# Kernel optimization log

Measured on AMD Instinct MI355X. Metric: run time of the kernel, lower is better.

The kernel has to match this reference:

```python
import jax, jax.numpy as jnp
import numpy as np

N_NODES, N_EDGES, N_GRAPHS = 100000, 1600000, 1000
DIN, DMID, DGLOB, DOUT = 128, 128, 64, 2


def setup_inputs() -> dict:
    key = jax.random.key(0)
    ks = jax.random.split(key, 12)
    x = jax.random.normal(ks[0], (N_NODES, DIN), dtype=jnp.float32)
    edge_index = jax.random.randint(ks[1], (2, N_EDGES), 0, N_NODES, dtype=jnp.int64 if jax.config.jax_enable_x64 else jnp.int32)
    u = jax.random.normal(ks[2], (N_GRAPHS, DGLOB), dtype=jnp.float32)
    batch = jnp.sort(jax.random.randint(ks[3], (N_NODES,), 0, N_GRAPHS))
    s = 1.0 / np.sqrt(DMID)
    W1 = jax.random.normal(ks[4], (DIN, DMID), dtype=jnp.float32) * s
    b1 = jnp.zeros((DMID,), dtype=jnp.float32)
    W2 = jax.random.normal(ks[5], (DMID, DMID), dtype=jnp.float32) * s
    b2 = jnp.zeros((DMID,), dtype=jnp.float32)
    Wh1 = jax.random.normal(ks[6], (DMID + DGLOB, DMID), dtype=jnp.float32) * s
    bh1 = jnp.zeros((DMID,), dtype=jnp.float32)
    Wh2 = jax.random.normal(ks[7], (DMID, DOUT), dtype=jnp.float32) * s
    bh2 = jnp.zeros((DOUT,), dtype=jnp.float32)
    return {"x": x, "edge_index": edge_index, "u": u, "batch": batch,
            "batch_size": N_GRAPHS, "W1": W1, "b1": b1, "W2": W2, "b2": b2,
            "Wh1": Wh1, "bh1": bh1, "Wh2": Wh2, "bh2": bh2}


def _gcn_conv(x, W, b, row, col, norm, n):
    # PyG GCNConv: linear transform then symmetric-normalized scatter-add
    h = x @ W                                    # [N, dmid]
    msg = norm[:, None] * h[row]                 # gather along source nodes
    out = jax.ops.segment_sum(msg, col, num_segments=n)  # scatter to dst
    return out + b


def reference(x, edge_index, u, batch, batch_size, W1, b1, W2, b2, Wh1, bh1, Wh2, bh2):
    n = x.shape[0]
    # add self-loops (GCNConv default, edge_weight=None -> all-ones weights)
    loop = jnp.arange(n, dtype=edge_index.dtype)
    row = jnp.concatenate([edge_index[0], loop])
    col = jnp.concatenate([edge_index[1], loop])
    deg = jax.ops.segment_sum(jnp.ones_like(col, dtype=x.dtype), col, num_segments=n)
    dinv = jnp.where(deg > 0, jax.lax.rsqrt(jnp.maximum(deg, 1e-12)), 0.0)
    norm = dinv[row] * dinv[col]                 # D^-1/2 A D^-1/2, shared by both layers

    h = jax.nn.relu(_gcn_conv(x, W1, b1, row, col, norm, n))
    h = jax.nn.relu(_gcn_conv(h, W2, b2, row, col, norm, n))

    # mean pool per graph
    sums = jax.ops.segment_sum(h, batch, num_segments=batch_size)
    cnt = jax.ops.segment_sum(jnp.ones((n,), dtype=h.dtype), batch, num_segments=batch_size)
    graph_emb = sums / jnp.maximum(cnt, 1.0)[:, None]

    hcat = jnp.concatenate([graph_emb, u], axis=-1)
    # head MLP (dropout in eval mode = identity)
    out = jax.nn.relu(hcat @ Wh1 + bh1) @ Wh2 + bh2
    return out
```

## Files before the change

### kernel.cpp

```cpp
#include <hip/hip_runtime.h>
#include <hip/hip_bf16.h>

#define NN 100000
#define NE 1600000
#define NG 1000
#define NBK 196
#define BSH 9
#define SLOT 10240
#define SLOTC 12288

typedef short short8 __attribute__((ext_vector_type(8)));
typedef float f32x4 __attribute__((ext_vector_type(4)));
typedef float f32x2 __attribute__((ext_vector_type(2)));

static inline int cdiv(int a, int b) { return (a + b - 1) / b; }

__device__ __forceinline__ unsigned short f2b(float f) {
    unsigned int u = __float_as_uint(f);
    u += 0x7fff + ((u >> 16) & 1);
    return (unsigned short)(u >> 16);
}
__device__ __forceinline__ unsigned int pack2(float lo, float hi) {
    return (unsigned int)f2b(lo) | ((unsigned int)f2b(hi) << 16);
}

template <int W>
__device__ __forceinline__ f32x2 f8_2f(unsigned int v) {
    return __builtin_amdgcn_cvt_pk_f32_fp8((int)v, W);
}
__device__ __forceinline__ unsigned int f2f8_lo(float a, float b, unsigned int old) {
    return (unsigned int)__builtin_amdgcn_cvt_pk_fp8_f32(a, b, (int)old, false);
}
__device__ __forceinline__ unsigned int f2f8_hi(float a, float b, unsigned int old) {
    return (unsigned int)__builtin_amdgcn_cvt_pk_fp8_f32(a, b, (int)old, true);
}
__device__ __forceinline__ unsigned char f2f8s(float a) {
    return (unsigned char)(__builtin_amdgcn_cvt_pk_fp8_f32(a, a, 0, false) & 0xFF);
}

__global__ __launch_bounds__(256) void k_prep(const float* __restrict__ W1,
                                              const float* __restrict__ W2,
                                              const float* __restrict__ b1,
                                              const float* __restrict__ b2,
                                              unsigned short* __restrict__ Wt1,
                                              unsigned char* __restrict__ Wt2p,
                                              float* __restrict__ b1p,
                                              float* __restrict__ b2p,
                                              int* __restrict__ gcur,
                                              const int* __restrict__ batch,
                                              int* __restrict__ gstart,
                                              unsigned char* __restrict__ Hs8,
                                              unsigned char* __restrict__ Hg2) {
    int b = blockIdx.x, t = threadIdx.x;
    if (b < 128) {
        if (t < 128) {
            Wt1[b * 128 + t] = f2b(W1[t * 128 + b]);
        } else {
            int q = t - 128;
            int c = (q & 7) * 16 + (q >> 3);
            Wt2p[b * 128 + q] = f2f8s(W2[c * 128 + b]);
        }
    } else if (b == 128) {
        if (t < NBK) gcur[t] = t * SLOT;
        if (t < 128) {
            int c = (t & 7) * 16 + (t >> 3);
            b1p[t] = b1[c];
            b2p[t] = b2[c];
        }
        if (t >= 128 && t < 136) {
            uint4 z; z.x = 0u; z.y = 0u; z.z = 0u; z.w = 0u;
            ((uint4*)(Hs8 + (size_t)NN * 128))[t - 128] = z;
        }
        if (t >= 136 && t < 144) {
            uint4 z; z.x = 0u; z.y = 0u; z.z = 0u; z.w = 0u;
            ((uint4*)(Hg2 + (size_t)NN * 128))[t - 136] = z;
        }
    } else {
        int n = (b - 129) * 256 + t;
        if (n <= NN) {
            int cur = (n == NN) ? NG : batch[n];
            int prev = (n == 0) ? -1 : batch[n - 1];
            for (int g = prev + 1; g <= cur; g++) gstart[g] = n;
        }
    }
}

__global__ __launch_bounds__(256) void k_bin2(const int* __restrict__ row,
                                              const int* __restrict__ col,
                                              int* __restrict__ gcur,
                                              unsigned int* __restrict__ tmp) {
    __shared__ unsigned int ent[4000];
    __shared__ unsigned int srt[4000];
    __shared__ unsigned char bkt[4000];
    __shared__ unsigned char bky[4000];
    __shared__ int cnt[NBK];
    __shared__ int gbase[NBK];
    __shared__ int lbase[NBK];
    __shared__ int sh[256];
    int t = threadIdx.x;
    if (t < NBK) cnt[t] = 0;
    __syncthreads();
    const int q0 = blockIdx.x * 1000;
    const int4* col4 = (const int4*)col;
    const int4* row4 = (const int4*)row;
#pragma unroll
    for (int it = 0; it < 4; it++) {
        int idx = it * 256 + t;
        if (idx < 1000) {
            int4 c = col4[q0 + idx];
            int4 r = row4[q0 + idx];
            int d, b;
            d = c.x; b = d >> BSH; atomicAdd(&cnt[b], 1);
            ent[idx * 4 + 0] = ((unsigned int)(d & 511) << 17) | (unsigned int)r.x;
            bkt[idx * 4 + 0] = (unsigned char)b;
            d = c.y; b = d >> BSH; atomicAdd(&cnt[b], 1);
            ent[idx * 4 + 1] = ((unsigned int)(d & 511) << 17) | (unsigned int)r.y;
            bkt[idx * 4 + 1] = (unsigned char)b;
            d = c.z; b = d >> BSH; atomicAdd(&cnt[b], 1);
            ent[idx * 4 + 2] = ((unsigned int)(d & 511) << 17) | (unsigned int)r.z;
            bkt[idx * 4 + 2] = (unsigned char)b;
            d = c.w; b = d >> BSH; atomicAdd(&cnt[b], 1);
            ent[idx * 4 + 3] = ((unsigned int)(d & 511) << 17) | (unsigned int)r.w;
            bkt[idx * 4 + 3] = (unsigned char)b;
        }
    }
    __syncthreads();
    int v = (t < NBK) ? cnt[t] : 0;
    sh[t] = v;
    __syncthreads();
    for (int d = 1; d < 256; d <<= 1) {
        int u = (t >= d) ? sh[t - d] : 0;
        __syncthreads();
        sh[t] += u;
        __syncthreads();
    }
    if (t < NBK) {
        lbase[t] = sh[t] - v;
        gbase[t] = atomicAdd(&gcur[t], v);
        cnt[t] = sh[t] - v;
    }
    __syncthreads();
#pragma unroll
    for (int it = 0; it < 16; it++) {
        int i = it * 256 + t;
        if (i < 4000) {
            int b = bkt[i];
            int p = atomicAdd(&cnt[b], 1);
            srt[p] = ent[i];
            bky[p] = (unsigned char)b;
        }
    }
    __syncthreads();
#pragma unroll
    for (int it = 0; it < 16; it++) {
        int i = it * 256 + t;
        if (i < 4000) {
            int b = bky[i];
            tmp[gbase[b] + (i - lbase[b])] = srt[i];
        }
    }
}

__global__ __launch_bounds__(1024) void k_bucket(const unsigned int* __restrict__ tmp,
                                                 const int* __restrict__ gcur,
                                                 unsigned int* __restrict__ meta,
                                                 float* __restrict__ dinv,
                                                 int* __restrict__ csr_src) {
    __shared__ unsigned int sent[SLOT];
    __shared__ int cnt[512];
    __shared__ int loff[512];
    __shared__ int send[512];
    __shared__ int sh[256];
    int b = blockIdx.x, t = threadIdx.x;
    int j0 = b << BSH;
    int nd = min(512, NN - j0);
    int rb = b * SLOT;
    int rbc = b * SLOTC;
    int m = gcur[b] - rb;
    if (t < 512) cnt[t] = 0;
    __syncthreads();
    for (int i = t; i < m; i += 1024) {
        unsigned int e = tmp[rb + i];
        sent[i] = e;
        atomicAdd(&cnt[e >> 17], 1);
    }
    __syncthreads();
    int r0 = 0, r1 = 0, p0 = 0, ts = 0;
    if (t < 256) {
        r0 = cnt[2 * t]; r1 = cnt[2 * t + 1];
        p0 = (r0 + 7) & ~7;
        int p1 = (r1 + 7) & ~7;
        ts = p0 + p1;
        sh[t] = ts;
    }
    __syncthreads();
    for (int d = 1; d < 256; d <<= 1) {
        int u = (t >= d && t < 256) ? sh[t - d] : 0;
        __syncthreads();
        if (t < 256) sh[t] += u;
        __syncthreads();
    }
    if (t < 256) {
        int ex = sh[t] - ts;
        loff[2 * t] = ex;
        loff[2 * t + 1] = ex + p0;
    }
    __syncthreads();
    for (int j = t; j < nd; j += 1024) {
        int o = rbc + loff[j];
        int dg = cnt[j];
        int dgp = (dg + 7) & ~7;
        meta[j0 + j] = (unsigned int)o | ((unsigned int)dgp << 22);
        send[j] = o + dgp;
        dinv[j0 + j] = rsqrtf((float)(dg + 1));
        cnt[j] = o;
    }
    __syncthreads();
    for (int i = t; i < m; i += 1024) {
        unsigned int e = sent[i];
        int d = e >> 17;
        int s = (int)(e & 0x1FFFFu);
        int p = atomicAdd(&cnt[d], 1);
        csr_src[p] = s;
    }
    __syncthreads();
    for (int j = t; j < nd; j += 1024) {
        int pe = send[j];
        for (int p = cnt[j]; p < pe; p++) csr_src[p] = NN;
    }
}

__global__ __launch_bounds__(256) void k_gemm1(const float* __restrict__ X,
                                               const unsigned short* __restrict__ Wt,
                                               const float* __restrict__ dinv,
                                               unsigned char* __restrict__ Hs8) {
    __shared__ __align__(16) unsigned short Ws[128 * 128];
    int t = threadIdx.x;
#pragma unroll
    for (int i = 0; i < 8; i++) {
        int id = t + i * 256;
        int n = id >> 4, c = id & 15;
        *(short8*)((char*)Ws + n * 256 + ((c ^ (n & 15)) << 4)) =
            *(const short8*)(Wt + n * 128 + c * 8);
    }
    __syncthreads();

    int lane = t & 63, wid = t >> 6;
    int n16 = lane & 15, quad = lane >> 4;
    int row_base = blockIdx.x * 128 + wid * 32;

    short8 a[2][4];
#pragma unroll
    for (int rt = 0; rt < 2; rt++) {
        int r = row_base + rt * 16 + n16;
        if (r > NN - 1) r = NN - 1;
        const float* ap = X + (size_t)r * 128 + quad * 8;
#pragma unroll
        for (int ks = 0; ks < 4; ks++) {
            float4 v0 = *(const float4*)(ap + ks * 32);
            float4 v1 = *(const float4*)(ap + ks * 32 + 4);
            uint4 up;
            up.x = pack2(v0.x, v0.y); up.y = pack2(v0.z, v0.w);
            up.z = pack2(v1.x, v1.y); up.w = pack2(v1.z, v1.w);
            a[rt][ks] = *(short8*)&up;
        }
    }

    f32x4 acc[2][8];
#pragma unroll
    for (int rt = 0; rt < 2; rt++)
#pragma unroll
        for (int ct = 0; ct < 8; ct++)
            acc[rt][ct] = (f32x4){0.f, 0.f, 0.f, 0.f};

#pragma unroll
    for (int ks = 0; ks < 4; ks++) {
#pragma unroll
        for (int ct = 0; ct < 8; ct++) {
            short8 b = *(const short8*)((const char*)Ws +
                        (ct * 16 + n16) * 256 + ((((ks << 2) + quad) ^ n16) << 4));
            acc[0][ct] = __builtin_amdgcn_mfma_f32_16x16x32_bf16(a[0][ks], b, acc[0][ct], 0, 0, 0);
            acc[1][ct] = __builtin_amdgcn_mfma_f32_16x16x32_bf16(a[1][ks], b, acc[1][ct], 0, 0, 0);
        }
    }

#pragma unroll
    for (int rt = 0; rt < 2; rt++) {
#pragma unroll
        for (int reg = 0; reg < 4; reg++) {
            int row = row_base + rt * 16 + quad * 4 + reg;
            if (row < NN) {
                float di = dinv[row];
                unsigned int u0 = 0, u1 = 0;
                u0 = f2f8_lo(acc[rt][0][reg] * di, acc[rt][1][reg] * di, u0);
                u0 = f2f8_hi(acc[rt][2][reg] * di, acc[rt][3][reg] * di, u0);
                u1 = f2f8_lo(acc[rt][4][reg] * di, acc[rt][5][reg] * di, u1);
                u1 = f2f8_hi(acc[rt][6][reg] * di, acc[rt][7][reg] * di, u1);
                uint2 o; o.x = u0; o.y = u1;
                ((uint2*)(Hs8 + (size_t)row * 128))[n16] = o;
            }
        }
    }
}

template <int FUSE>
__global__ __launch_bounds__(256) void k_agg(const unsigned char* __restrict__ Hb,
                                             const unsigned int* __restrict__ meta,
                                             const int* __restrict__ csr_src,
                                             const float* __restrict__ dinv,
                                             const float* __restrict__ biasp,
                                             const unsigned char* __restrict__ Wt2p,
                                             unsigned char* __restrict__ outp) {
    __shared__ __align__(16) unsigned char sm[FUSE ? (128 * 128 + 16 * 128) : 16];
    int t = threadIdx.x;
    if (FUSE) {
#pragma unroll
        for (int i = 0; i < 8; i++) {
            int id = t + i * 256;
            int n = id >> 4, c = id & 15;
            *(uint2*)(sm + n * 128 + ((c ^ (n & 15)) << 3)) =
                *(const uint2*)(Wt2p + n * 128 + c * 8);
        }
    }
    int sub = t >> 4;
    int node = blockIdx.x * 16 + sub;
    int li = t & 15;
    unsigned lo8 = (unsigned)li * 8u;
    unsigned int md = meta[node];
    int base = (int)(md & 0x3FFFFFu);
    int degp = (int)(md >> 22);
    f32x2 A0 = {0.f, 0.f}, A1 = {0.f, 0.f}, A2 = {0.f, 0.f}, A3 = {0.f, 0.f};
#define LDH(idx) (*(const uint2*)(Hb + (unsigned)(idx) * 128u + lo8))
#define ACC8(V) { \
        A0 += f8_2f<0>((V).x); A1 += f8_2f<1>((V).x); \
        A2 += f8_2f<0>((V).y); A3 += f8_2f<1>((V).y); }
    uint2 v = LDH(node);
    const int4* ip = (const int4*)(csr_src + base);
    int4 i0 = ip[0], i1 = ip[1], i2 = ip[2], i3 = ip[3];
    ACC8(v)
    for (int e0 = 0; e0 < degp; e0 += 16) {
        uint2 w0 = LDH(i0.x), w1 = LDH(i0.y), w2 = LDH(i0.z), w3 = LDH(i0.w);
        uint2 w4 = LDH(i1.x), w5 = LDH(i1.y), w6 = LDH(i1.z), w7 = LDH(i1.w);
        uint2 w8 = {0, 0}, w9 = {0, 0}, wA = {0, 0}, wB = {0, 0};
        uint2 wC = {0, 0}, wD = {0, 0}, wE = {0, 0}, wF = {0, 0};
        if (e0 + 8 < degp) {
            w8 = LDH(i2.x); w9 = LDH(i2.y); wA = LDH(i2.z); wB = LDH(i2.w);
            wC = LDH(i3.x); wD = LDH(i3.y); wE = LDH(i3.z); wF = LDH(i3.w);
        }
        if (e0 + 16 < degp) {
            const int4* np = (const int4*)(csr_src + base + e0 + 16);
            i0 = np[0]; i1 = np[1]; i2 = np[2]; i3 = np[3];
        }
        ACC8(w0) ACC8(w1) ACC8(w2) ACC8(w3)
        ACC8(w4) ACC8(w5) ACC8(w6) ACC8(w7)
        ACC8(w8) ACC8(w9) ACC8(wA) ACC8(wB)
        ACC8(wC) ACC8(wD) ACC8(wE) ACC8(wF)
    }
#undef ACC8
#undef LDH
    float di = dinv[node];
    const float4* b4 = (const float4*)biasp;
    float4 bA = b4[li * 2], bB = b4[li * 2 + 1];
    float r0 = fmaxf(fmaf(di, A0[0], bA.x), 0.f);
    float r1 = fmaxf(fmaf(di, A0[1], bA.y), 0.f);
    float r2 = fmaxf(fmaf(di, A1[0], bA.z), 0.f);
    float r3 = fmaxf(fmaf(di, A1[1], bA.w), 0.f);
    float r4 = fmaxf(fmaf(di, A2[0], bB.x), 0.f);
    float r5 = fmaxf(fmaf(di, A2[1], bB.y), 0.f);
    float r6 = fmaxf(fmaf(di, A3[0], bB.z), 0.f);
    float r7 = fmaxf(fmaf(di, A3[1], bB.w), 0.f);
    unsigned int u0 = 0, u1 = 0;
    u0 = f2f8_lo(r0, r1, u0); u0 = f2f8_hi(r2, r3, u0);
    u1 = f2f8_lo(r4, r5, u1); u1 = f2f8_hi(r6, r7, u1);
    uint2 o; o.x = u0; o.y = u1;
    if (!FUSE) {
        *(uint2*)(outp + (unsigned)node * 128u + lo8) = o;
        return;
    }
    *(uint2*)(sm + 16384 + sub * 128 + (((li ^ sub) & 15) << 3)) = o;
    __syncthreads();
    if (t < 64) {
        int n16 = t & 15, quad = t >> 4;
        f32x4 acc[8];
#pragma unroll
        for (int ct = 0; ct < 8; ct++) acc[ct] = (f32x4){0.f, 0.f, 0.f, 0.f};
#pragma unroll
        for (int ks = 0; ks < 4; ks++) {
            uint2 av = *(const uint2*)(sm + 16384 + n16 * 128 +
                                       ((((ks << 2) + quad) ^ n16) << 3));
            long aa = __builtin_bit_cast(long, av);
#pragma unroll
            for (int ct = 0; ct < 8; ct++) {
                uint2 bv = *(const uint2*)(sm + (ct * 16 + n16) * 128 +
                                           ((((ks << 2) + quad) ^ n16) << 3));
                long bb = __builtin_bit_cast(long, bv);
                acc[ct] = __builtin_amdgcn_mfma_f32_16x16x32_fp8_fp8(aa, bb, acc[ct], 0, 0, 0);
            }
        }
#pragma unroll
        for (int reg = 0; reg < 4; reg++) {
            int row = blockIdx.x * 16 + quad * 4 + reg;
            float d2 = dinv[row];
            unsigned int g0 = 0, g1 = 0;
            g0 = f2f8_lo(acc[0][reg] * d2, acc[1][reg] * d2, g0);
            g0 = f2f8_hi(acc[2][reg] * d2, acc[3][reg] * d2, g0);
            g1 = f2f8_lo(acc[4][reg] * d2, acc[5][reg] * d2, g1);
            g1 = f2f8_hi(acc[6][reg] * d2, acc[7][reg] * d2, g1);
            uint2 go; go.x = g0; go.y = g1;
            ((uint2*)(outp + (size_t)row * 128))[n16] = go;
        }
    }
}

__global__ __launch_bounds__(256) void k_poolhead(const unsigned char* __restrict__ A,
                                                  const int* __restrict__ gstart,
                                                  const float* __restrict__ u,
                                                  const float* __restrict__ Wh1,
                                                  const float* __restrict__ bh1,
                                                  const float* __restrict__ Wh2,
                                                  const float* __restrict__ bh2,
                                                  float* __restrict__ out) {
    int g = blockIdx.x, t = threadIdx.x;
    int start = gstart[g];
    int end = gstart[g + 1];

    int li = t & 7;
    int ri = t >> 3;
    float acc[16];
#pragma unroll
    for (int j = 0; j < 16; j++) acc[j] = 0.f;
    f32x2 p;
    for (int i = start + ri; i < end; i += 32) {
        uint4 v = ((const uint4*)A)[(size_t)i * 8 + li];
#define UP(VV, base) p = f8_2f<0>(VV); acc[base] += p.x; acc[base+1] += p.y; \
                     p = f8_2f<1>(VV); acc[base+2] += p.x; acc[base+3] += p.y;
        UP(v.x, 0) UP(v.y, 4) UP(v.z, 8) UP(v.w, 12)
#undef UP
    }
#pragma unroll
    for (int j = 0; j < 16; j++) {
        acc[j] += __shfl_xor(acc[j], 8);
        acc[j] += __shfl_xor(acc[j], 16);
        acc[j] += __shfl_xor(acc[j], 32);
    }
    __shared__ float part[4][128];
    __shared__ float hc[192];
    __shared__ float tt[128];
    __shared__ float red[8];
    int w = t >> 6;
    if ((t & 63) < 8) {
#pragma unroll
        for (int j = 0; j < 16; j++) part[w][li * 16 + j] = acc[j];
    }
    __syncthreads();
    float cntf = (float)max(end - start, 1);
    if (t < 128) {
        int q = (t & 15) * 8 + (t >> 4);
        hc[t] = (part[0][q] + part[1][q] + part[2][q] + part[3][q]) / cntf;
    } else if (t < 192) {
        hc[t] = u[g * 64 + (t - 128)];
    }
    __syncthreads();
    if (t < 128) {
        float a2 = bh1[t];
#pragma unroll 8
        for (int k = 0; k < 192; k++) a2 = fmaf(hc[k], Wh1[k * 128 + t], a2);
        tt[t] = fmaxf(a2, 0.f);
    }
    __syncthreads();
    float p0 = 0.f, p1 = 0.f;
    if (t < 128) {
        float vv = tt[t];
        p0 = vv * Wh2[t * 2];
        p1 = vv * Wh2[t * 2 + 1];
    }
#pragma unroll
    for (int d = 32; d >= 1; d >>= 1) {
        p0 += __shfl_xor(p0, d);
        p1 += __shfl_xor(p1, d);
    }
    if ((t & 63) == 0) { red[w * 2] = p0; red[w * 2 + 1] = p1; }
    __syncthreads();
    if (t == 0) out[g * 2 + 0] = bh2[0] + red[0] + red[2];
    if (t == 1) out[g * 2 + 1] = bh2[1] + red[1] + red[3];
}

extern "C" void kernel_launch(void* const* d_in, const int* in_sizes, int n_in,
                              void* d_out, int out_size, void* d_ws, size_t ws_size,
                              hipStream_t stream) {
    const float* x   = (const float*)d_in[0];
    const int*   ei  = (const int*)d_in[1];
    const int*   row = ei;
    const int*   col = ei + NE;
    const float* u   = (const float*)d_in[2];
    const int*   batch = (const int*)d_in[3];
    const float* W1  = (const float*)d_in[5];
    const float* b1  = (const float*)d_in[6];
    const float* W2  = (const float*)d_in[7];
    const float* b2  = (const float*)d_in[8];
    const float* Wh1 = (const float*)d_in[9];
    const float* bh1 = (const float*)d_in[10];
    const float* Wh2 = (const float*)d_in[11];
    const float* bh2 = (const float*)d_in[12];
    float* out = (float*)d_out;

    char* ws = (char*)d_ws;
    size_t o = 0;
    auto alloc = [&](size_t bytes) -> void* {
        void* p = ws + o;
        o += (bytes + 511) & ~(size_t)511;
        return p;
    };
    unsigned char*  Hs8 = (unsigned char*)alloc((size_t)(NN + 1) * 128);
    unsigned char*  Hg2 = (unsigned char*)alloc((size_t)(NN + 1) * 128);
    unsigned char*  A2b = (unsigned char*)alloc((size_t)NN * 128);
    unsigned short* Wt1 = (unsigned short*)alloc((size_t)128 * 128 * 2);
    unsigned char*  Wt2p= (unsigned char*)alloc((size_t)128 * 128);
    float* b1p    = (float*)alloc((size_t)128 * 4);
    float* b2p    = (float*)alloc((size_t)128 * 4);
    float* dinv   = (float*)alloc((size_t)NN * 4);
    unsigned int* meta = (unsigned int*)alloc((size_t)NN * 4);
    int*   csr_src= (int*)alloc((size_t)NBK * SLOTC * 4 + 512);
    unsigned int* tmp = (unsigned int*)alloc((size_t)NBK * SLOT * 4);
    int*   gcur   = (int*)alloc((size_t)256 * 4);
    int*   gstart = (int*)alloc((size_t)(NG + 1) * 4);

    k_prep<<<129 + cdiv(NN + 1, 256), 256, 0, stream>>>(W1, W2, b1, b2, Wt1, Wt2p,
                                                        b1p, b2p, gcur, batch, gstart,
                                                        Hs8, Hg2);
    k_bin2<<<400, 256, 0, stream>>>(row, col, gcur, tmp);
    k_bucket<<<NBK, 1024, 0, stream>>>(tmp, gcur, meta, dinv, csr_src);

    k_gemm1<<<cdiv(NN, 128), 256, 0, stream>>>(x, Wt1, dinv, Hs8);
    k_agg<1><<<NN / 16, 256, 0, stream>>>(Hs8, meta, csr_src, dinv, b1p, Wt2p, Hg2);
    k_agg<0><<<NN / 16, 256, 0, stream>>>(Hg2, meta, csr_src, dinv, b2p, nullptr, A2b);

    k_poolhead<<<NG, 256, 0, stream>>>(A2b, gstart, u, Wh1, bh1, Wh2, bh2, out);
}
```

Baseline: 232.6 us.

## Restructure aggregation kernels with wider per-lane loads and per-wave fused GEMM

The fused aggregation kernel now gives each node 4 lanes (32 bytes each) instead of 16 lanes of 8 bytes. Each wave owns a 16-node tile and runs its own MFMA GEMM against W2, reading W2 straight from global memory with only a wave barrier, so the block-wide LDS staging of W2 and the __syncthreads are gone. The second aggregation uses 8 lanes per node with 16-byte loads and an 8-edge unroll. This cuts memory instructions per gathered row and removes the serialized single-wave GEMM tail, at the cost of fewer lanes in flight per node and more registers. It also assumes the padded CSR degrees are multiples of 4 and 8.

```diff
diff --git a/kernel.cpp b/kernel.cpp
--- a/kernel.cpp
+++ b/kernel.cpp
@@ -303,103 +303,91 @@
     }
 }
 
-template <int FUSE>
-__global__ __launch_bounds__(256) void k_agg(const unsigned char* __restrict__ Hb,
-                                             const unsigned int* __restrict__ meta,
-                                             const int* __restrict__ csr_src,
-                                             const float* __restrict__ dinv,
-                                             const float* __restrict__ biasp,
-                                             const unsigned char* __restrict__ Wt2p,
-                                             unsigned char* __restrict__ outp) {
-    __shared__ __align__(16) unsigned char sm[FUSE ? (128 * 128 + 16 * 128) : 16];
+__global__ __launch_bounds__(256) void k_aggf(const unsigned char* __restrict__ Hb,
+                                              const unsigned int* __restrict__ meta,
+                                              const int* __restrict__ csr_src,
+                                              const float* __restrict__ dinv,
+                                              const float* __restrict__ biasp,
+                                              const unsigned char* __restrict__ Wt2p,
+                                              unsigned char* __restrict__ outp) {
+    __shared__ __align__(16) unsigned char At[4][16 * 128];
     int t = threadIdx.x;
-    if (FUSE) {
-#pragma unroll
-        for (int i = 0; i < 8; i++) {
-            int id = t + i * 256;
-            int n = id >> 4, c = id & 15;
-            *(uint2*)(sm + n * 128 + ((c ^ (n & 15)) << 3)) =
-                *(const uint2*)(Wt2p + n * 128 + c * 8);
-        }
-    }
-    int sub = t >> 4;
-    int node = blockIdx.x * 16 + sub;
-    int li = t & 15;
-    unsigned lo8 = (unsigned)li * 8u;
+    int wid = t >> 6, lane = t & 63;
+    int ns = lane >> 2, li4 = lane & 3;
+    int tile0 = blockIdx.x * 64 + wid * 16;
+    int node = tile0 + ns;
+    if (node > NN - 1) node = NN - 1;
     unsigned int md = meta[node];
     int base = (int)(md & 0x3FFFFFu);
     int degp = (int)(md >> 22);
-    f32x2 A0 = {0.f, 0.f}, A1 = {0.f, 0.f}, A2 = {0.f, 0.f}, A3 = {0.f, 0.f};
-#define LDH(idx) (*(const uint2*)(Hb + (unsigned)(idx) * 128u + lo8))
-#define ACC8(V) { \
-        A0 += f8_2f<0>((V).x); A1 += f8_2f<1>((V).x); \
-        A2 += f8_2f<0>((V).y); A3 += f8_2f<1>((V).y); }
-    uint2 v = LDH(node);
-    const int4* ip = (const int4*)(csr_src + base);
-    int4 i0 = ip[0], i1 = ip[1], i2 = ip[2], i3 = ip[3];
-    ACC8(v)
-    for (int e0 = 0; e0 < degp; e0 += 16) {
-        uint2 w0 = LDH(i0.x), w1 = LDH(i0.y), w2 = LDH(i0.z), w3 = LDH(i0.w);
-        uint2 w4 = LDH(i1.x), w5 = LDH(i1.y), w6 = LDH(i1.z), w7 = LDH(i1.w);
-        uint2 w8 = {0, 0}, w9 = {0, 0}, wA = {0, 0}, wB = {0, 0};
-        uint2 wC = {0, 0}, wD = {0, 0}, wE = {0, 0}, wF = {0, 0};
-        if (e0 + 8 < degp) {
-            w8 = LDH(i2.x); w9 = LDH(i2.y); wA = LDH(i2.z); wB = LDH(i2.w);
-            wC = LDH(i3.x); wD = LDH(i3.y); wE = LDH(i3.z); wF = LDH(i3.w);
-        }
-        if (e0 + 16 < degp) {
-            const int4* np = (const int4*)(csr_src + base + e0 + 16);
-            i0 = np[0]; i1 = np[1]; i2 = np[2]; i3 = np[3];
-        }
-        ACC8(w0) ACC8(w1) ACC8(w2) ACC8(w3)
-        ACC8(w4) ACC8(w5) ACC8(w6) ACC8(w7)
-        ACC8(w8) ACC8(w9) ACC8(wA) ACC8(wB)
-        ACC8(wC) ACC8(wD) ACC8(wE) ACC8(wF)
-    }
-#undef ACC8
-#undef LDH
+    f32x2 A[16];
+#pragma unroll
+    for (int j = 0; j < 16; j++) A[j] = (f32x2){0.f, 0.f};
+    const unsigned char* hl = Hb + (unsigned)li4 * 32u;
+#define LD4(idx, half) (*(const uint4*)(hl + (unsigned)(idx) * 128u + (half) * 16u))
+#define ACC16(lo, hi) { \
+    A[0] += f8_2f<0>((lo).x); A[1] += f8_2f<1>((lo).x); \
+    A[2] += f8_2f<0>((lo).y); A[3] += f8_2f<1>((lo).y); \
+    A[4] += f8_2f<0>((lo).z); A[5] += f8_2f<1>((lo).z); \
+    A[6] += f8_2f<0>((lo).w); A[7] += f8_2f<1>((lo).w); \
+    A[8] += f8_2f<0>((hi).x); A[9] += f8_2f<1>((hi).x); \
+    A[10] += f8_2f<0>((hi).y); A[11] += f8_2f<1>((hi).y); \
+    A[12] += f8_2f<0>((hi).z); A[13] += f8_2f<1>((hi).z); \
+    A[14] += f8_2f<0>((hi).w); A[15] += f8_2f<1>((hi).w); }
+    uint4 s0 = LD4(node, 0), s1 = LD4(node, 1);
+    int4 ix = *(const int4*)(csr_src + base);
+    ACC16(s0, s1)
+    for (int e0 = 0; e0 < degp; e0 += 4) {
+        uint4 l0 = LD4(ix.x, 0), h0 = LD4(ix.x, 1);
+        uint4 l1 = LD4(ix.y, 0), h1 = LD4(ix.y, 1);
+        uint4 l2 = LD4(ix.z, 0), h2 = LD4(ix.z, 1);
+        uint4 l3 = LD4(ix.w, 0), h3 = LD4(ix.w, 1);
+        ix = *(const int4*)(csr_src + base + e0 + 4);
+        ACC16(l0, h0) ACC16(l1, h1) ACC16(l2, h2) ACC16(l3, h3)
+    }
+#undef ACC16
+#undef LD4
     float di = dinv[node];
-    const float4* b4 = (const float4*)biasp;
-    float4 bA = b4[li * 2], bB = b4[li * 2 + 1];
-    float r0 = fmaxf(fmaf(di, A0[0], bA.x), 0.f);
-    float r1 = fmaxf(fmaf(di, A0[1], bA.y), 0.f);
-    float r2 = fmaxf(fmaf(di, A1[0], bA.z), 0.f);
-    float r3 = fmaxf(fmaf(di, A1[1], bA.w), 0.f);
-    float r4 = fmaxf(fmaf(di, A2[0], bB.x), 0.f);
-    float r5 = fmaxf(fmaf(di, A2[1], bB.y), 0.f);
-    float r6 = fmaxf(fmaf(di, A3[0], bB.z), 0.f);
-    float r7 = fmaxf(fmaf(di, A3[1], bB.w), 0.f);
-    unsigned int u0 = 0, u1 = 0;
-    u0 = f2f8_lo(r0, r1, u0); u0 = f2f8_hi(r2, r3, u0);
-    u1 = f2f8_lo(r4, r5, u1); u1 = f2f8_hi(r6, r7, u1);
-    uint2 o; o.x = u0; o.y = u1;
-    if (!FUSE) {
-        *(uint2*)(outp + (unsigned)node * 128u + lo8) = o;
-        return;
-    }
-    *(uint2*)(sm + 16384 + sub * 128 + (((li ^ sub) & 15) << 3)) = o;
-    __syncthreads();
-    if (t < 64) {
-        int n16 = t & 15, quad = t >> 4;
-        f32x4 acc[8];
-#pragma unroll
-        for (int ct = 0; ct < 8; ct++) acc[ct] = (f32x4){0.f, 0.f, 0.f, 0.f};
-#pragma unroll
-        for (int ks = 0; ks < 4; ks++) {
-            uint2 av = *(const uint2*)(sm + 16384 + n16 * 128 +
-                                       ((((ks << 2) + quad) ^ n16) << 3));
-            long aa = __builtin_bit_cast(long, av);
-#pragma unroll
-            for (int ct = 0; ct < 8; ct++) {
-                uint2 bv = *(const uint2*)(sm + (ct * 16 + n16) * 128 +
-                                           ((((ks << 2) + quad) ^ n16) << 3));
-                long bb = __builtin_bit_cast(long, bv);
-                acc[ct] = __builtin_amdgcn_mfma_f32_16x16x32_fp8_fp8(aa, bb, acc[ct], 0, 0, 0);
-            }
-        }
-#pragma unroll
-        for (int reg = 0; reg < 4; reg++) {
-            int row = blockIdx.x * 16 + quad * 4 + reg;
+    const f32x2* bp2 = (const f32x2*)biasp;
+    unsigned int w[8];
+#pragma unroll
+    for (int k = 0; k < 8; k++) {
+        f32x2 b0 = bp2[li4 * 16 + 2 * k], b1 = bp2[li4 * 16 + 2 * k + 1];
+        float r0 = fmaxf(fmaf(di, A[2 * k].x, b0.x), 0.f);
+        float r1 = fmaxf(fmaf(di, A[2 * k].y, b0.y), 0.f);
+        float r2 = fmaxf(fmaf(di, A[2 * k + 1].x, b1.x), 0.f);
+        float r3 = fmaxf(fmaf(di, A[2 * k + 1].y, b1.y), 0.f);
+        unsigned int u = f2f8_lo(r0, r1, 0);
+        w[k] = f2f8_hi(r2, r3, u);
+    }
+    unsigned char* Aw = At[wid];
+#pragma unroll
+    for (int m = 0; m < 4; m++) {
+        int c = li4 * 4 + m;
+        uint2 wp; wp.x = w[2 * m]; wp.y = w[2 * m + 1];
+        *(uint2*)(Aw + ns * 128 + (((c ^ ns) & 15) << 3)) = wp;
+    }
+    __builtin_amdgcn_wave_barrier();
+    int n16 = lane & 15, quad = lane >> 4;
+    f32x4 acc[8];
+#pragma unroll
+    for (int ct = 0; ct < 8; ct++) acc[ct] = (f32x4){0.f, 0.f, 0.f, 0.f};
+#pragma unroll
+    for (int ks = 0; ks < 4; ks++) {
+        uint2 av = *(const uint2*)(Aw + n16 * 128 + ((((ks << 2) + quad) ^ n16) << 3));
+        long aa = __builtin_bit_cast(long, av);
+#pragma unroll
+        for (int ct = 0; ct < 8; ct++) {
+            uint2 bv = *(const uint2*)(Wt2p + (ct * 16 + n16) * 128 +
+                                       (((ks << 2) + quad) << 3));
+            long bb = __builtin_bit_cast(long, bv);
+            acc[ct] = __builtin_amdgcn_mfma_f32_16x16x32_fp8_fp8(aa, bb, acc[ct], 0, 0, 0);
+        }
+    }
+#pragma unroll
+    for (int reg = 0; reg < 4; reg++) {
+        int row = tile0 + quad * 4 + reg;
+        if (row < NN) {
             float d2 = dinv[row];
             unsigned int g0 = 0, g1 = 0;
             g0 = f2f8_lo(acc[0][reg] * d2, acc[1][reg] * d2, g0);
@@ -410,6 +398,60 @@
             ((uint2*)(outp + (size_t)row * 128))[n16] = go;
         }
     }
+}
+
+__global__ __launch_bounds__(256) void k_agg2(const unsigned char* __restrict__ Hb,
+                                              const unsigned int* __restrict__ meta,
+                                              const int* __restrict__ csr_src,
+                                              const float* __restrict__ dinv,
+                                              const float* __restrict__ biasp,
+                                              unsigned char* __restrict__ outp) {
+    int t = threadIdx.x;
+    int lane = t & 63, wid = t >> 6;
+    int ns = lane >> 3, li8 = lane & 7;
+    int node = blockIdx.x * 32 + wid * 8 + ns;
+    unsigned int md = meta[node];
+    int base = (int)(md & 0x3FFFFFu);
+    int degp = (int)(md >> 22);
+    f32x2 A[8];
+#pragma unroll
+    for (int j = 0; j < 8; j++) A[j] = (f32x2){0.f, 0.f};
+    const unsigned char* hl = Hb + (unsigned)li8 * 16u;
+#define LD4B(idx) (*(const uint4*)(hl + (unsigned)(idx) * 128u))
+#define ACC8V(v) { \
+    A[0] += f8_2f<0>((v).x); A[1] += f8_2f<1>((v).x); \
+    A[2] += f8_2f<0>((v).y); A[3] += f8_2f<1>((v).y); \
+    A[4] += f8_2f<0>((v).z); A[5] += f8_2f<1>((v).z); \
+    A[6] += f8_2f<0>((v).w); A[7] += f8_2f<1>((v).w); }
+    uint4 sv = LD4B(node);
+    int4 ia = *(const int4*)(csr_src + base);
+    int4 ib = *(const int4*)(csr_src + base + 4);
+    ACC8V(sv)
+    for (int e0 = 0; e0 < degp; e0 += 8) {
+        uint4 w0 = LD4B(ia.x), w1 = LD4B(ia.y), w2 = LD4B(ia.z), w3 = LD4B(ia.w);
+        uint4 w4 = LD4B(ib.x), w5 = LD4B(ib.y), w6 = LD4B(ib.z), w7 = LD4B(ib.w);
+        ia = *(const int4*)(csr_src + base + e0 + 8);
+        ib = *(const int4*)(csr_src + base + e0 + 12);
+        ACC8V(w0) ACC8V(w1) ACC8V(w2) ACC8V(w3)
+        ACC8V(w4) ACC8V(w5) ACC8V(w6) ACC8V(w7)
+    }
+#undef ACC8V
+#undef LD4B
+    float di = dinv[node];
+    const f32x2* bp2 = (const f32x2*)biasp;
+    unsigned int w[4];
+#pragma unroll
+    for (int k = 0; k < 4; k++) {
+        f32x2 b0 = bp2[li8 * 8 + 2 * k], b1 = bp2[li8 * 8 + 2 * k + 1];
+        float r0 = fmaxf(fmaf(di, A[2 * k].x, b0.x), 0.f);
+        float r1 = fmaxf(fmaf(di, A[2 * k].y, b0.y), 0.f);
+        float r2 = fmaxf(fmaf(di, A[2 * k + 1].x, b1.x), 0.f);
+        float r3 = fmaxf(fmaf(di, A[2 * k + 1].y, b1.y), 0.f);
+        unsigned int u = f2f8_lo(r0, r1, 0);
+        w[k] = f2f8_hi(r2, r3, u);
+    }
+    uint4 o; o.x = w[0]; o.y = w[1]; o.z = w[2]; o.w = w[3];
+    *(uint4*)(outp + (unsigned)node * 128u + (unsigned)li8 * 16u) = o;
 }
 
 __global__ __launch_bounds__(256) void k_poolhead(const unsigned char* __restrict__ A,
@@ -532,8 +574,8 @@
     k_bucket<<<NBK, 1024, 0, stream>>>(tmp, gcur, meta, dinv, csr_src);
 
     k_gemm1<<<cdiv(NN, 128), 256, 0, stream>>>(x, Wt1, dinv, Hs8);
-    k_agg<1><<<NN / 16, 256, 0, stream>>>(Hs8, meta, csr_src, dinv, b1p, Wt2p, Hg2);
-    k_agg<0><<<NN / 16, 256, 0, stream>>>(Hg2, meta, csr_src, dinv, b2p, nullptr, A2b);
+    k_aggf<<<cdiv(NN, 64), 256, 0, stream>>>(Hs8, meta, csr_src, dinv, b1p, Wt2p, Hg2);
+    k_agg2<<<NN / 32, 256, 0, stream>>>(Hg2, meta, csr_src, dinv, b2p, A2b);
 
     k_poolhead<<<NG, 256, 0, stream>>>(A2b, gstart, u, Wh1, bh1, Wh2, bh2, out);
 }
```

Measured after the change: 260.8 us. 12.2% more time.

## Split fused layer-2 GEMM across all four waves and read weights from global

Applied to the files above, without the earlier changes.

The fused aggregation kernel no longer stages the full 128x128 fp8 weight matrix into shared memory for every 16-node block. All four waves now take part in the MFMA step, each computing two 16-column output tiles and loading weight fragments directly from global memory, where they should stay cache-resident. Results are repacked through a small shared buffer so the global store stays coalesced. This cuts shared memory per block from about 18KB to 4KB, which should raise occupancy, and removes the idle-wave serial tail. The cost is an extra barrier and more global or L2 weight traffic per block.

```diff
diff --git a/kernel.cpp b/kernel.cpp
--- a/kernel.cpp
+++ b/kernel.cpp
@@ -311,17 +311,8 @@
                                              const float* __restrict__ biasp,
                                              const unsigned char* __restrict__ Wt2p,
                                              unsigned char* __restrict__ outp) {
-    __shared__ __align__(16) unsigned char sm[FUSE ? (128 * 128 + 16 * 128) : 16];
+    __shared__ __align__(16) unsigned char sm[FUSE ? 4096 : 16];
     int t = threadIdx.x;
-    if (FUSE) {
-#pragma unroll
-        for (int i = 0; i < 8; i++) {
-            int id = t + i * 256;
-            int n = id >> 4, c = id & 15;
-            *(uint2*)(sm + n * 128 + ((c ^ (n & 15)) << 3)) =
-                *(const uint2*)(Wt2p + n * 128 + c * 8);
-        }
-    }
     int sub = t >> 4;
     int node = blockIdx.x * 16 + sub;
     int li = t & 15;
@@ -377,39 +368,38 @@
         *(uint2*)(outp + (unsigned)node * 128u + lo8) = o;
         return;
     }
-    *(uint2*)(sm + 16384 + sub * 128 + (((li ^ sub) & 15) << 3)) = o;
-    __syncthreads();
-    if (t < 64) {
-        int n16 = t & 15, quad = t >> 4;
-        f32x4 acc[8];
-#pragma unroll
-        for (int ct = 0; ct < 8; ct++) acc[ct] = (f32x4){0.f, 0.f, 0.f, 0.f};
-#pragma unroll
-        for (int ks = 0; ks < 4; ks++) {
-            uint2 av = *(const uint2*)(sm + 16384 + n16 * 128 +
-                                       ((((ks << 2) + quad) ^ n16) << 3));
-            long aa = __builtin_bit_cast(long, av);
-#pragma unroll
-            for (int ct = 0; ct < 8; ct++) {
-                uint2 bv = *(const uint2*)(sm + (ct * 16 + n16) * 128 +
-                                           ((((ks << 2) + quad) ^ n16) << 3));
-                long bb = __builtin_bit_cast(long, bv);
-                acc[ct] = __builtin_amdgcn_mfma_f32_16x16x32_fp8_fp8(aa, bb, acc[ct], 0, 0, 0);
-            }
-        }
-#pragma unroll
-        for (int reg = 0; reg < 4; reg++) {
-            int row = blockIdx.x * 16 + quad * 4 + reg;
-            float d2 = dinv[row];
-            unsigned int g0 = 0, g1 = 0;
-            g0 = f2f8_lo(acc[0][reg] * d2, acc[1][reg] * d2, g0);
-            g0 = f2f8_hi(acc[2][reg] * d2, acc[3][reg] * d2, g0);
-            g1 = f2f8_lo(acc[4][reg] * d2, acc[5][reg] * d2, g1);
-            g1 = f2f8_hi(acc[6][reg] * d2, acc[7][reg] * d2, g1);
-            uint2 go; go.x = g0; go.y = g1;
-            ((uint2*)(outp + (size_t)row * 128))[n16] = go;
-        }
-    }
+    *(uint2*)(sm + sub * 128 + (((li ^ sub) & 15) << 3)) = o;
+    __syncthreads();
+    int wid = t >> 6, lane = t & 63;
+    int n16 = lane & 15, quad = lane >> 4;
+    f32x4 acc[2];
+    acc[0] = (f32x4){0.f, 0.f, 0.f, 0.f};
+    acc[1] = (f32x4){0.f, 0.f, 0.f, 0.f};
+    int ct0 = wid * 2;
+#pragma unroll
+    for (int ks = 0; ks < 4; ks++) {
+        uint2 av = *(const uint2*)(sm + n16 * 128 + ((((ks << 2) + quad) ^ n16) << 3));
+        long aa = __builtin_bit_cast(long, av);
+#pragma unroll
+        for (int j = 0; j < 2; j++) {
+            uint2 bv = *(const uint2*)(Wt2p + ((ct0 + j) * 16 + n16) * 128 +
+                                       (((ks << 2) + quad) << 3));
+            long bb = __builtin_bit_cast(long, bv);
+            acc[j] = __builtin_amdgcn_mfma_f32_16x16x32_fp8_fp8(aa, bb, acc[j], 0, 0, 0);
+        }
+    }
+#pragma unroll
+    for (int reg = 0; reg < 4; reg++) {
+        int rl = quad * 4 + reg;
+        float d2 = dinv[blockIdx.x * 16 + rl];
+        unsigned int p = f2f8_lo(acc[0][reg] * d2, acc[1][reg] * d2, 0);
+        *(unsigned short*)(sm + 2048 + rl * 128 + n16 * 8 + wid * 2) =
+            (unsigned short)(p & 0xFFFFu);
+    }
+    __syncthreads();
+    int rr = t >> 4, cc = t & 15;
+    uint2 go = *(const uint2*)(sm + 2048 + rr * 128 + cc * 8);
+    *(uint2*)(outp + (size_t)(blockIdx.x * 16 + rr) * 128 + cc * 8) = go;
 }
 
 __global__ __launch_bounds__(256) void k_poolhead(const unsigned char* __restrict__ A,
```

New measurement: 244.7 us. 5.2% more time.
